# Kernel optimization log

Hardware: AMD Instinct MI355X
Metric: run time of the kernel (lower is better)

Reference implementation:

```python
import jax, jax.numpy as jnp
import numpy as np

EPS = 1e-5

def _weight_quant(w):
    # BitNet b1.58: per-tensor ternary quantization with STE.
    scale = 1.0 / jnp.maximum(jnp.mean(jnp.abs(w)), EPS)
    wq = jnp.clip(jnp.round(w * scale), -1.0, 1.0) / scale
    return w + jax.lax.stop_gradient(wq - w)

def _act_quant(x):
    # per-token int8 absmax quantization with STE.
    scale = 127.0 / jnp.maximum(jnp.max(jnp.abs(x), axis=-1, keepdims=True), EPS)
    xq = jnp.clip(jnp.round(x * scale), -128.0, 127.0) / scale
    return x + jax.lax.stop_gradient(xq - x)

def _bitlinear(x, w):
    # x: [..., in], w: [out, in] (torch layout)
    return jnp.einsum('bsd,hd->bsh', _act_quant(x), _weight_quant(w))

def setup_inputs() -> dict:
    key = jax.random.key(0)
    k1, k2, k3, k4 = jax.random.split(key, 4)
    B, S, D, H = 4, 2048, 2048, 5632
    x = jax.random.normal(k1, (B, S, D), dtype=jnp.float32)
    w1 = jax.random.normal(k2, (H, D), dtype=jnp.float32) * 0.02
    w2 = jax.random.normal(k3, (H, D), dtype=jnp.float32) * 0.02
    w3 = jax.random.normal(k4, (D, H), dtype=jnp.float32) * 0.02
    return {"x": x, "w1": w1, "w2": w2, "w3": w3}

def reference(x, w1, w2, w3):
    gate = jax.nn.silu(_bitlinear(x, w1))   # [B,S,H]
    up = _bitlinear(x, w2)                  # [B,S,H]
    h = gate * up                           # [B,S,H]
    return _bitlinear(h, w3)                # [B,S,D]
```

## Files before the change

kernel.cpp:

```cpp
#include <hip/hip_runtime.h>
#include <hip/hip_bf16.h>
#include <math.h>

#define EPSQ 1e-5f

typedef __attribute__((ext_vector_type(4))) int i32x4;

__device__ __forceinline__ void gload_lds16(const void* g, void* l) {
  __builtin_amdgcn_global_load_lds(
      (__attribute__((address_space(1))) void*)g,
      (__attribute__((address_space(3))) void*)l, 16, 0, 0);
}

__device__ __forceinline__ int clampi8(float v, float lo, float hi) {
  return (int)rintf(fminf(hi, fmaxf(lo, v)));
}

__global__ void wabs_kernel(const float* __restrict__ w, int n4, double* __restrict__ sum) {
  __shared__ double sm[256];
  const float4* w4 = (const float4*)w;
  double acc = 0.0;
  const int stride = gridDim.x * blockDim.x;
  for (int i = blockIdx.x * blockDim.x + threadIdx.x; i < n4; i += stride) {
    float4 v = w4[i];
    acc += (double)fabsf(v.x) + (double)fabsf(v.y) + (double)fabsf(v.z) + (double)fabsf(v.w);
  }
  sm[threadIdx.x] = acc;
  __syncthreads();
  for (int s = 128; s > 0; s >>= 1) {
    if ((int)threadIdx.x < s) sm[threadIdx.x] += sm[threadIdx.x + s];
    __syncthreads();
  }
  if (threadIdx.x == 0) atomicAdd(sum, sm[0]);
}

__global__ void wquant_kernel(const float* __restrict__ w, int n4,
                              const double* __restrict__ sum, double inv_n,
                              unsigned int* __restrict__ wq) {
  const float s = (float)fmax(*sum * inv_n, (double)EPSQ);
  const float scale = 1.0f / s;
  const int i = blockIdx.x * blockDim.x + threadIdx.x;
  if (i >= n4) return;
  float4 v = ((const float4*)w)[i];
  const int b0 = clampi8(rintf(v.x * scale), -1.f, 1.f);
  const int b1 = clampi8(rintf(v.y * scale), -1.f, 1.f);
  const int b2 = clampi8(rintf(v.z * scale), -1.f, 1.f);
  const int b3 = clampi8(rintf(v.w * scale), -1.f, 1.f);
  wq[i] = (unsigned int)((b0 & 0xff) | ((b1 & 0xff) << 8) |
                         ((b2 & 0xff) << 16) | ((b3 & 0xff) << 24));
}

__global__ void aquant_kernel(const float* __restrict__ x, int K,
                              unsigned char* __restrict__ q, float* __restrict__ arow) {
  const int row = blockIdx.x;
  const int n4 = K >> 2;
  const float4* xr = (const float4*)(x + (size_t)row * K);
  float m = 0.f;
  for (int c = threadIdx.x; c < n4; c += blockDim.x) {
    float4 v = xr[c];
    m = fmaxf(m, fmaxf(fmaxf(fabsf(v.x), fabsf(v.y)), fmaxf(fabsf(v.z), fabsf(v.w))));
  }
  __shared__ float sm[256];
  sm[threadIdx.x] = m;
  __syncthreads();
  for (int s = 128; s > 0; s >>= 1) {
    if ((int)threadIdx.x < s) sm[threadIdx.x] = fmaxf(sm[threadIdx.x], sm[threadIdx.x + s]);
    __syncthreads();
  }
  const float mv = fmaxf(sm[0], EPSQ);
  const float scale = 127.0f / mv;
  if (threadIdx.x == 0) arow[row] = mv * (1.0f / 127.0f);
  unsigned int* qr = (unsigned int*)(q + (size_t)row * K);
  for (int c = threadIdx.x; c < n4; c += blockDim.x) {
    float4 v = xr[c];
    const int b0 = clampi8(v.x * scale, -128.f, 127.f);
    const int b1 = clampi8(v.y * scale, -128.f, 127.f);
    const int b2 = clampi8(v.z * scale, -128.f, 127.f);
    const int b3 = clampi8(v.w * scale, -128.f, 127.f);
    qr[c] = (unsigned int)((b0 & 0xff) | ((b1 & 0xff) << 8) |
                           ((b2 & 0xff) << 16) | ((b3 & 0xff) << 24));
  }
}

#define BM 128
#define BN 128
#define BKI 64

__launch_bounds__(256, 2)
__global__ void gemm_gateup(const unsigned char* __restrict__ Aq,
                            const unsigned char* __restrict__ W1q,
                            const unsigned char* __restrict__ W2q,
                            const float* __restrict__ arow,
                            const double* __restrict__ wsum,
                            float* __restrict__ Hbuf,
                            const int N, const int K) {
  __shared__ __align__(16) unsigned char lA[BM * BKI];
  __shared__ __align__(16) unsigned char lB1[BN * BKI];
  __shared__ __align__(16) unsigned char lB2[BN * BKI];

  const int tid = threadIdx.x;
  const int lane = tid & 63;
  const int wid = tid >> 6;
  const int wm = wid >> 1, wn = wid & 1;
  const int m0 = blockIdx.y * BM;
  const int n0 = blockIdx.x * BN;

  const double inv_n = 1.0 / 11534336.0;
  const float sw1 = (float)fmax(wsum[0] * inv_n, (double)EPSQ);
  const float sw2 = (float)fmax(wsum[1] * inv_n, (double)EPSQ);

  i32x4 acc1[4][4] = {};
  i32x4 acc2[4][4] = {};

  const int so = wid * 2048;
  const unsigned char* Ab  = Aq  + (size_t)m0 * K;
  const unsigned char* B1b = W1q + (size_t)n0 * K;
  const unsigned char* B2b = W2q + (size_t)n0 * K;

  for (int k0 = 0; k0 < K; k0 += BKI) {
#pragma unroll
    for (int t = 0; t < 2; ++t) {
      const int o = so + t * 1024 + lane * 16;
      const int r = o >> 6;
      const int cb = o & 63;
      const size_t goff = (size_t)r * K + (size_t)k0 + (size_t)cb;
      gload_lds16(Ab  + goff, (char*)lA  + so + t * 1024);
      gload_lds16(B1b + goff, (char*)lB1 + so + t * 1024);
      gload_lds16(B2b + goff, (char*)lB2 + so + t * 1024);
    }
    __syncthreads();

    const unsigned char* pa  = lA  + (wm * 64 + (lane & 15)) * BKI + (lane >> 4) * 16;
    const unsigned char* pb1 = lB1 + (wn * 64 + (lane & 15)) * BKI + (lane >> 4) * 16;
    const unsigned char* pb2 = lB2 + (wn * 64 + (lane & 15)) * BKI + (lane >> 4) * 16;
    i32x4 af[4];
#pragma unroll
    for (int i = 0; i < 4; ++i) af[i] = *(const i32x4*)(pa + i * 16 * BKI);
#pragma unroll
    for (int j = 0; j < 4; ++j) {
      i32x4 b1 = *(const i32x4*)(pb1 + j * 16 * BKI);
      i32x4 b2 = *(const i32x4*)(pb2 + j * 16 * BKI);
#pragma unroll
      for (int i = 0; i < 4; ++i) {
        acc1[i][j] = __builtin_amdgcn_mfma_i32_16x16x64_i8(af[i], b1, acc1[i][j], 0, 0, 0);
        acc2[i][j] = __builtin_amdgcn_mfma_i32_16x16x64_i8(af[i], b2, acc2[i][j], 0, 0, 0);
      }
    }
    __syncthreads();
  }

#pragma unroll
  for (int i = 0; i < 4; ++i) {
    const int rb = m0 + wm * 64 + i * 16 + (lane >> 4) * 4;
#pragma unroll
    for (int qe = 0; qe < 4; ++qe) {
      const int grow = rb + qe;
      const float a = arow[grow];
      const float f1 = a * sw1;
      const float f2 = a * sw2;
      float* hr = Hbuf + (size_t)grow * N + n0 + wn * 64 + (lane & 15);
#pragma unroll
      for (int j = 0; j < 4; ++j) {
        const float y1 = (float)acc1[i][j][qe] * f1;
        const float y2 = (float)acc2[i][j][qe] * f2;
        const float g = y1 / (1.0f + expf(-y1));
        hr[j * 16] = g * y2;
      }
    }
  }
}

__launch_bounds__(256, 2)
__global__ void gemm_down(const unsigned char* __restrict__ Aq,
                          const unsigned char* __restrict__ Wq,
                          const float* __restrict__ arow,
                          const double* __restrict__ wsum,
                          float* __restrict__ Out,
                          const int N, const int K) {
  __shared__ __align__(16) unsigned char lA[BM * BKI];
  __shared__ __align__(16) unsigned char lB[BN * BKI];

  const int tid = threadIdx.x;
  const int lane = tid & 63;
  const int wid = tid >> 6;
  const int wm = wid >> 1, wn = wid & 1;
  const int m0 = blockIdx.y * BM;
  const int n0 = blockIdx.x * BN;

  const double inv_n = 1.0 / 11534336.0;
  const float sw3 = (float)fmax(wsum[2] * inv_n, (double)EPSQ);

  i32x4 acc[4][4] = {};

  const int so = wid * 2048;
  const unsigned char* Ab = Aq + (size_t)m0 * K;
  const unsigned char* Bb = Wq + (size_t)n0 * K;

  for (int k0 = 0; k0 < K; k0 += BKI) {
#pragma unroll
    for (int t = 0; t < 2; ++t) {
      const int o = so + t * 1024 + lane * 16;
      const int r = o >> 6;
      const int cb = o & 63;
      const size_t goff = (size_t)r * K + (size_t)k0 + (size_t)cb;
      gload_lds16(Ab + goff, (char*)lA + so + t * 1024);
      gload_lds16(Bb + goff, (char*)lB + so + t * 1024);
    }
    __syncthreads();

    const unsigned char* pa = lA + (wm * 64 + (lane & 15)) * BKI + (lane >> 4) * 16;
    const unsigned char* pb = lB + (wn * 64 + (lane & 15)) * BKI + (lane >> 4) * 16;
    i32x4 af[4];
#pragma unroll
    for (int i = 0; i < 4; ++i) af[i] = *(const i32x4*)(pa + i * 16 * BKI);
#pragma unroll
    for (int j = 0; j < 4; ++j) {
      i32x4 b = *(const i32x4*)(pb + j * 16 * BKI);
#pragma unroll
      for (int i = 0; i < 4; ++i) {
        acc[i][j] = __builtin_amdgcn_mfma_i32_16x16x64_i8(af[i], b, acc[i][j], 0, 0, 0);
      }
    }
    __syncthreads();
  }

#pragma unroll
  for (int i = 0; i < 4; ++i) {
    const int rb = m0 + wm * 64 + i * 16 + (lane >> 4) * 4;
#pragma unroll
    for (int qe = 0; qe < 4; ++qe) {
      const int grow = rb + qe;
      const float f = arow[grow] * sw3;
      float* orow = Out + (size_t)grow * N + n0 + wn * 64 + (lane & 15);
#pragma unroll
      for (int j = 0; j < 4; ++j) {
        orow[j * 16] = (float)acc[i][j][qe] * f;
      }
    }
  }
}

extern "C" void kernel_launch(void* const* d_in, const int* in_sizes, int n_in,
                              void* d_out, int out_size, void* d_ws, size_t ws_size,
                              hipStream_t stream) {
  (void)n_in; (void)out_size;
  const float* x  = (const float*)d_in[0];
  const float* w1 = (const float*)d_in[1];
  const float* w2 = (const float*)d_in[2];
  const float* w3 = (const float*)d_in[3];
  float* out = (float*)d_out;

  const int D = 2048, H = 5632;
  const int M = in_sizes[0] / D;
  const long long NW = (long long)H * D;

  auto al = [](size_t v) { return (v + 255) & ~(size_t)255; };

  size_t off = 0;
  const size_t o_wsum = off; off += al(3 * sizeof(double));
  const size_t o_w1q  = off; off += al((size_t)NW);
  const size_t o_w2q  = off; off += al((size_t)NW);
  const size_t o_w3q  = off; off += al((size_t)NW);
  const size_t fixed = off;

  int Mc = 128;
  for (int cand = M; cand >= 128; cand >>= 1) {
    size_t need = fixed
                + al((size_t)cand * 4)
                + al((size_t)cand * 4)
                + al((size_t)cand * D)
                + al((size_t)cand * H * 4)
                + al((size_t)cand * H);
    if (need <= ws_size) { Mc = cand; break; }
  }

  size_t coff = fixed;
  const size_t o_arow1 = coff; coff += al((size_t)Mc * 4);
  const size_t o_arow2 = coff; coff += al((size_t)Mc * 4);
  const size_t o_qx    = coff; coff += al((size_t)Mc * D);
  const size_t o_hbuf  = coff; coff += al((size_t)Mc * H * 4);
  const size_t o_qh    = coff; coff += al((size_t)Mc * H);

  char* ws = (char*)d_ws;
  double* wsum        = (double*)(ws + o_wsum);
  unsigned char* w1q  = (unsigned char*)(ws + o_w1q);
  unsigned char* w2q  = (unsigned char*)(ws + o_w2q);
  unsigned char* w3q  = (unsigned char*)(ws + o_w3q);
  float* arow1        = (float*)(ws + o_arow1);
  float* arow2        = (float*)(ws + o_arow2);
  unsigned char* qx   = (unsigned char*)(ws + o_qx);
  float* hbuf         = (float*)(ws + o_hbuf);
  unsigned char* qh   = (unsigned char*)(ws + o_qh);

  hipMemsetAsync(wsum, 0, 3 * sizeof(double), stream);

  const int n4w = (int)(NW / 4);
  wabs_kernel<<<2048, 256, 0, stream>>>(w1, n4w, wsum + 0);
  wabs_kernel<<<2048, 256, 0, stream>>>(w2, n4w, wsum + 1);
  wabs_kernel<<<2048, 256, 0, stream>>>(w3, n4w, wsum + 2);

  const double inv_n = 1.0 / (double)NW;
  wquant_kernel<<<n4w / 256, 256, 0, stream>>>(w1, n4w, wsum + 0, inv_n, (unsigned int*)w1q);
  wquant_kernel<<<n4w / 256, 256, 0, stream>>>(w2, n4w, wsum + 1, inv_n, (unsigned int*)w2q);
  wquant_kernel<<<n4w / 256, 256, 0, stream>>>(w3, n4w, wsum + 2, inv_n, (unsigned int*)w3q);

  for (int c = 0; c < M; c += Mc) {
    aquant_kernel<<<Mc, 256, 0, stream>>>(x + (size_t)c * D, D, qx, arow1);
    gemm_gateup<<<dim3(H / BN, Mc / BM), 256, 0, stream>>>(qx, w1q, w2q, arow1, wsum,
                                                           hbuf, H, D);
    aquant_kernel<<<Mc, 256, 0, stream>>>(hbuf, H, qh, arow2);
    gemm_down<<<dim3(D / BN, Mc / BM), 256, 0, stream>>>(qh, w3q, arow2, wsum,
                                                         out + (size_t)c * D, D, H);
  }
}
```

Before: 581.8 us.

## Triple-buffer int8 GEMMs with swizzled LDS, larger tiles and block remapping

Both int8 MFMA GEMMs now use 512-thread blocks over 256x128 tiles. K tiles are staged through a three-slot LDS ring, so global-to-LDS loads for tile t+2 overlap MFMA work on tile t, synchronised with vmcnt waits and raw barriers instead of two __syncthreads per step. LDS chunks are XOR-swizzled to reduce bank conflicts, and the 1D grid is remapped in groups of eight blocks to improve L2 reuse. The trade-off is more LDS per block, which may limit occupancy, plus a minimum row chunk of 256.

```diff
diff --git a/kernel.cpp b/kernel.cpp
--- a/kernel.cpp
+++ b/kernel.cpp
@@ -82,73 +82,121 @@
   }
 }
 
-#define BM 128
-#define BN 128
-#define BKI 64
-
-__launch_bounds__(256, 2)
+#define BKP 64
+
+
+#define PIPE_BARRIER(N)                                         \
+  asm volatile("s_waitcnt vmcnt(" #N ")" ::: "memory");         \
+  __builtin_amdgcn_s_barrier();                                 \
+  asm volatile("" ::: "memory");
+
+#define GU_SLOT 32768
+
+__launch_bounds__(512, 2)
 __global__ void gemm_gateup(const unsigned char* __restrict__ Aq,
                             const unsigned char* __restrict__ W1q,
                             const unsigned char* __restrict__ W2q,
                             const float* __restrict__ arow,
                             const double* __restrict__ wsum,
                             float* __restrict__ Hbuf,
-                            const int N, const int K) {
-  __shared__ __align__(16) unsigned char lA[BM * BKI];
-  __shared__ __align__(16) unsigned char lB1[BN * BKI];
-  __shared__ __align__(16) unsigned char lB2[BN * BKI];
+                            const int N, const int K,
+                            const int MBb, const int NBb) {
+  __shared__ char lds[3 * GU_SLOT];
 
   const int tid = threadIdx.x;
   const int lane = tid & 63;
   const int wid = tid >> 6;
-  const int wm = wid >> 1, wn = wid & 1;
-  const int m0 = blockIdx.y * BM;
-  const int n0 = blockIdx.x * BN;
+  const int wm = wid >> 1;
+  const int wn = wid & 1;
+
+  const int total = MBb * NBb;
+  int swz = blockIdx.x;
+  if ((total & 7) == 0) swz = (swz & 7) * (total >> 3) + (swz >> 3);
+  const int nb = swz % NBb;
+  const int mb = swz / NBb;
+  const int m0 = mb * 256;
+  const int n0 = nb * 128;
+
+  const unsigned char* Ab  = Aq  + (size_t)m0 * K;
+  const unsigned char* B1b = W1q + (size_t)n0 * K;
+  const unsigned char* B2b = W2q + (size_t)n0 * K;
+
+  auto stage = [&](int kt, int s) {
+    const int k0 = kt * BKP;
+    char* base = lds + s * GU_SLOT;
+#pragma unroll
+    for (int is = 0; is < 2; ++is) {
+      const int p = is * 8192 + wid * 1024 + lane * 16;
+      const int r = p >> 6;
+      const int c = ((p >> 4) & 3) ^ ((r >> 1) & 3);
+      gload_lds16(Ab + (size_t)r * K + k0 + c * 16, base + is * 8192 + wid * 1024);
+    }
+    {
+      const int p = wid * 1024 + lane * 16;
+      const int r = p >> 6;
+      const int c = ((p >> 4) & 3) ^ ((r >> 1) & 3);
+      const size_t go = (size_t)r * K + k0 + c * 16;
+      gload_lds16(B1b + go, base + 16384 + wid * 1024);
+      gload_lds16(B2b + go, base + 24576 + wid * 1024);
+    }
+  };
+
+  const int c16 = lane >> 4;
+  int offA[4], offB1[4], offB2[4];
+#pragma unroll
+  for (int i = 0; i < 4; ++i) {
+    const int row = wm * 64 + i * 16 + (lane & 15);
+    offA[i] = row * 64 + ((c16 ^ ((row >> 1) & 3)) << 4);
+  }
+#pragma unroll
+  for (int j = 0; j < 4; ++j) {
+    const int n = wn * 64 + j * 16 + (lane & 15);
+    const int o = n * 64 + ((c16 ^ ((n >> 1) & 3)) << 4);
+    offB1[j] = 16384 + o;
+    offB2[j] = 24576 + o;
+  }
+
+  i32x4 acc1[4][4] = {};
+  i32x4 acc2[4][4] = {};
+
+  const int NT = K / BKP;
+  stage(0, 0);
+  stage(1, 1);
+  PIPE_BARRIER(4)
+
+  int s = 0, s2 = 2;
+  for (int t = 0; t < NT; ++t) {
+    if (t + 2 < NT) stage(t + 2, s2);
+    const char* sb = lds + s * GU_SLOT;
+    i32x4 af[4], b1f[4], b2f[4];
+#pragma unroll
+    for (int i = 0; i < 4; ++i) af[i] = *(const i32x4*)(sb + offA[i]);
+#pragma unroll
+    for (int j = 0; j < 4; ++j) {
+      b1f[j] = *(const i32x4*)(sb + offB1[j]);
+      b2f[j] = *(const i32x4*)(sb + offB2[j]);
+    }
+    __builtin_amdgcn_s_setprio(1);
+#pragma unroll
+    for (int j = 0; j < 4; ++j)
+#pragma unroll
+      for (int i = 0; i < 4; ++i) {
+        acc1[i][j] = __builtin_amdgcn_mfma_i32_16x16x64_i8(af[i], b1f[j], acc1[i][j], 0, 0, 0);
+        acc2[i][j] = __builtin_amdgcn_mfma_i32_16x16x64_i8(af[i], b2f[j], acc2[i][j], 0, 0, 0);
+      }
+    __builtin_amdgcn_s_setprio(0);
+    if (t + 2 < NT) {
+      PIPE_BARRIER(4)
+    } else if (t + 1 < NT) {
+      PIPE_BARRIER(0)
+    }
+    s = (s == 2) ? 0 : s + 1;
+    s2 = (s2 == 2) ? 0 : s2 + 1;
+  }
 
   const double inv_n = 1.0 / 11534336.0;
   const float sw1 = (float)fmax(wsum[0] * inv_n, (double)EPSQ);
   const float sw2 = (float)fmax(wsum[1] * inv_n, (double)EPSQ);
-
-  i32x4 acc1[4][4] = {};
-  i32x4 acc2[4][4] = {};
-
-  const int so = wid * 2048;
-  const unsigned char* Ab  = Aq  + (size_t)m0 * K;
-  const unsigned char* B1b = W1q + (size_t)n0 * K;
-  const unsigned char* B2b = W2q + (size_t)n0 * K;
-
-  for (int k0 = 0; k0 < K; k0 += BKI) {
-#pragma unroll
-    for (int t = 0; t < 2; ++t) {
-      const int o = so + t * 1024 + lane * 16;
-      const int r = o >> 6;
-      const int cb = o & 63;
-      const size_t goff = (size_t)r * K + (size_t)k0 + (size_t)cb;
-      gload_lds16(Ab  + goff, (char*)lA  + so + t * 1024);
-      gload_lds16(B1b + goff, (char*)lB1 + so + t * 1024);
-      gload_lds16(B2b + goff, (char*)lB2 + so + t * 1024);
-    }
-    __syncthreads();
-
-    const unsigned char* pa  = lA  + (wm * 64 + (lane & 15)) * BKI + (lane >> 4) * 16;
-    const unsigned char* pb1 = lB1 + (wn * 64 + (lane & 15)) * BKI + (lane >> 4) * 16;
-    const unsigned char* pb2 = lB2 + (wn * 64 + (lane & 15)) * BKI + (lane >> 4) * 16;
-    i32x4 af[4];
-#pragma unroll
-    for (int i = 0; i < 4; ++i) af[i] = *(const i32x4*)(pa + i * 16 * BKI);
-#pragma unroll
-    for (int j = 0; j < 4; ++j) {
-      i32x4 b1 = *(const i32x4*)(pb1 + j * 16 * BKI);
-      i32x4 b2 = *(const i32x4*)(pb2 + j * 16 * BKI);
-#pragma unroll
-      for (int i = 0; i < 4; ++i) {
-        acc1[i][j] = __builtin_amdgcn_mfma_i32_16x16x64_i8(af[i], b1, acc1[i][j], 0, 0, 0);
-        acc2[i][j] = __builtin_amdgcn_mfma_i32_16x16x64_i8(af[i], b2, acc2[i][j], 0, 0, 0);
-      }
-    }
-    __syncthreads();
-  }
-
 #pragma unroll
   for (int i = 0; i < 4; ++i) {
     const int rb = m0 + wm * 64 + i * 16 + (lane >> 4) * 4;
@@ -163,67 +211,106 @@
       for (int j = 0; j < 4; ++j) {
         const float y1 = (float)acc1[i][j][qe] * f1;
         const float y2 = (float)acc2[i][j][qe] * f2;
-        const float g = y1 / (1.0f + expf(-y1));
-        hr[j * 16] = g * y2;
+        hr[j * 16] = (y1 / (1.0f + expf(-y1))) * y2;
       }
     }
   }
 }
 
-__launch_bounds__(256, 2)
+#define DN_SLOT 24576
+
+__launch_bounds__(512, 2)
 __global__ void gemm_down(const unsigned char* __restrict__ Aq,
                           const unsigned char* __restrict__ Wq,
                           const float* __restrict__ arow,
                           const double* __restrict__ wsum,
                           float* __restrict__ Out,
-                          const int N, const int K) {
-  __shared__ __align__(16) unsigned char lA[BM * BKI];
-  __shared__ __align__(16) unsigned char lB[BN * BKI];
+                          const int N, const int K,
+                          const int MBb, const int NBb) {
+  __shared__ char lds[3 * DN_SLOT];
 
   const int tid = threadIdx.x;
   const int lane = tid & 63;
   const int wid = tid >> 6;
-  const int wm = wid >> 1, wn = wid & 1;
-  const int m0 = blockIdx.y * BM;
-  const int n0 = blockIdx.x * BN;
+  const int wm = wid >> 1;
+  const int wn = wid & 1;
+
+  const int total = MBb * NBb;
+  int swz = blockIdx.x;
+  if ((total & 7) == 0) swz = (swz & 7) * (total >> 3) + (swz >> 3);
+  const int nb = swz % NBb;
+  const int mb = swz / NBb;
+  const int m0 = mb * 256;
+  const int n0 = nb * 128;
+
+  const unsigned char* Ab = Aq + (size_t)m0 * K;
+  const unsigned char* Bb = Wq + (size_t)n0 * K;
+
+  auto stage = [&](int kt, int s) {
+    const int k0 = kt * BKP;
+    char* base = lds + s * DN_SLOT;
+#pragma unroll
+    for (int is = 0; is < 2; ++is) {
+      const int p = is * 8192 + wid * 1024 + lane * 16;
+      const int r = p >> 6;
+      const int c = ((p >> 4) & 3) ^ ((r >> 1) & 3);
+      gload_lds16(Ab + (size_t)r * K + k0 + c * 16, base + is * 8192 + wid * 1024);
+    }
+    {
+      const int p = wid * 1024 + lane * 16;
+      const int r = p >> 6;
+      const int c = ((p >> 4) & 3) ^ ((r >> 1) & 3);
+      gload_lds16(Bb + (size_t)r * K + k0 + c * 16, base + 16384 + wid * 1024);
+    }
+  };
+
+  const int c16 = lane >> 4;
+  int offA[4], offB[4];
+#pragma unroll
+  for (int i = 0; i < 4; ++i) {
+    const int row = wm * 64 + i * 16 + (lane & 15);
+    offA[i] = row * 64 + ((c16 ^ ((row >> 1) & 3)) << 4);
+  }
+#pragma unroll
+  for (int j = 0; j < 4; ++j) {
+    const int n = wn * 64 + j * 16 + (lane & 15);
+    offB[j] = 16384 + n * 64 + ((c16 ^ ((n >> 1) & 3)) << 4);
+  }
+
+  i32x4 acc[4][4] = {};
+
+  const int NT = K / BKP;
+  stage(0, 0);
+  stage(1, 1);
+  PIPE_BARRIER(3)
+
+  int s = 0, s2 = 2;
+  for (int t = 0; t < NT; ++t) {
+    if (t + 2 < NT) stage(t + 2, s2);
+    const char* sb = lds + s * DN_SLOT;
+    i32x4 af[4], bf[4];
+#pragma unroll
+    for (int i = 0; i < 4; ++i) af[i] = *(const i32x4*)(sb + offA[i]);
+#pragma unroll
+    for (int j = 0; j < 4; ++j) bf[j] = *(const i32x4*)(sb + offB[j]);
+    __builtin_amdgcn_s_setprio(1);
+#pragma unroll
+    for (int j = 0; j < 4; ++j)
+#pragma unroll
+      for (int i = 0; i < 4; ++i)
+        acc[i][j] = __builtin_amdgcn_mfma_i32_16x16x64_i8(af[i], bf[j], acc[i][j], 0, 0, 0);
+    __builtin_amdgcn_s_setprio(0);
+    if (t + 2 < NT) {
+      PIPE_BARRIER(3)
+    } else if (t + 1 < NT) {
+      PIPE_BARRIER(0)
+    }
+    s = (s == 2) ? 0 : s + 1;
+    s2 = (s2 == 2) ? 0 : s2 + 1;
+  }
 
   const double inv_n = 1.0 / 11534336.0;
   const float sw3 = (float)fmax(wsum[2] * inv_n, (double)EPSQ);
-
-  i32x4 acc[4][4] = {};
-
-  const int so = wid * 2048;
-  const unsigned char* Ab = Aq + (size_t)m0 * K;
-  const unsigned char* Bb = Wq + (size_t)n0 * K;
-
-  for (int k0 = 0; k0 < K; k0 += BKI) {
-#pragma unroll
-    for (int t = 0; t < 2; ++t) {
-      const int o = so + t * 1024 + lane * 16;
-      const int r = o >> 6;
-      const int cb = o & 63;
-      const size_t goff = (size_t)r * K + (size_t)k0 + (size_t)cb;
-      gload_lds16(Ab + goff, (char*)lA + so + t * 1024);
-      gload_lds16(Bb + goff, (char*)lB + so + t * 1024);
-    }
-    __syncthreads();
-
-    const unsigned char* pa = lA + (wm * 64 + (lane & 15)) * BKI + (lane >> 4) * 16;
-    const unsigned char* pb = lB + (wn * 64 + (lane & 15)) * BKI + (lane >> 4) * 16;
-    i32x4 af[4];
-#pragma unroll
-    for (int i = 0; i < 4; ++i) af[i] = *(const i32x4*)(pa + i * 16 * BKI);
-#pragma unroll
-    for (int j = 0; j < 4; ++j) {
-      i32x4 b = *(const i32x4*)(pb + j * 16 * BKI);
-#pragma unroll
-      for (int i = 0; i < 4; ++i) {
-        acc[i][j] = __builtin_amdgcn_mfma_i32_16x16x64_i8(af[i], b, acc[i][j], 0, 0, 0);
-      }
-    }
-    __syncthreads();
-  }
-
 #pragma unroll
   for (int i = 0; i < 4; ++i) {
     const int rb = m0 + wm * 64 + i * 16 + (lane >> 4) * 4;
@@ -263,8 +350,8 @@
   const size_t o_w3q  = off; off += al((size_t)NW);
   const size_t fixed = off;
 
-  int Mc = 128;
-  for (int cand = M; cand >= 128; cand >>= 1) {
+  int Mc = 256;
+  for (int cand = M; cand >= 256; cand >>= 1) {
     size_t need = fixed
                 + al((size_t)cand * 4)
                 + al((size_t)cand * 4)
@@ -304,12 +391,15 @@
   wquant_kernel<<<n4w / 256, 256, 0, stream>>>(w2, n4w, wsum + 1, inv_n, (unsigned int*)w2q);
   wquant_kernel<<<n4w / 256, 256, 0, stream>>>(w3, n4w, wsum + 2, inv_n, (unsigned int*)w3q);
 
+  const int NBgu = H / 128;
+  const int NBdn = D / 128;
   for (int c = 0; c < M; c += Mc) {
+    const int MBb = Mc / 256;
     aquant_kernel<<<Mc, 256, 0, stream>>>(x + (size_t)c * D, D, qx, arow1);
-    gemm_gateup<<<dim3(H / BN, Mc / BM), 256, 0, stream>>>(qx, w1q, w2q, arow1, wsum,
-                                                           hbuf, H, D);
+    gemm_gateup<<<MBb * NBgu, 512, 0, stream>>>(qx, w1q, w2q, arow1, wsum,
+                                                hbuf, H, D, MBb, NBgu);
     aquant_kernel<<<Mc, 256, 0, stream>>>(hbuf, H, qh, arow2);
-    gemm_down<<<dim3(D / BN, Mc / BM), 256, 0, stream>>>(qh, w3q, arow2, wsum,
-                                                         out + (size_t)c * D, D, H);
-  }
-}
+    gemm_down<<<MBb * NBdn, 512, 0, stream>>>(qh, w3q, arow2, wsum,
+                                              out + (size_t)c * D, D, H, MBb, NBdn);
+  }
+}
```

Result: faster. 532.3 us (-8.5%).
